# Optimization experiments

Hardware: AMD Instinct MI355X
Metric: run time of the kernel (lower is better)

## Reference

```python
import jax, jax.numpy as jnp
import numpy as np

TLEN, BSZ, HID = 64, 32, 1024
SLEN = 200
V_TGT = 32000
V_EXT = 2000
UNK = 0  # ext_dict UNK index, ignored in the onehot scatter


def setup_inputs() -> dict:
    key = jax.random.key(0)
    ks = jax.random.split(key, 6)
    hidden = jax.random.normal(ks[0], (TLEN, BSZ, HID), dtype=jnp.float32)
    attn = jax.random.uniform(ks[1], (TLEN, BSZ, SLEN), dtype=jnp.float32)
    attn = attn / jnp.sum(attn, axis=-1, keepdims=True)  # attention-like distribution
    copy_to_ext = jax.random.randint(ks[2], (SLEN, BSZ), 0, V_EXT)
    W_out = jax.random.normal(ks[3], (V_TGT, HID), dtype=jnp.float32) * 0.02
    b_out = jnp.zeros((V_TGT,), dtype=jnp.float32)
    w_copy = jax.random.normal(ks[4], (1, HID), dtype=jnp.float32) * 0.02
    b_copy = jnp.zeros((1,), dtype=jnp.float32)
    return {"hidden": hidden, "attn": attn, "copy_to_ext": copy_to_ext,
            "W_out": W_out, "b_out": b_out, "w_copy": w_copy, "b_copy": b_copy}


def _safe_log(v):
    return jnp.log(jnp.clip(v, 0.001, 1.0 - 0.001))


def reference(hidden, attn, copy_to_ext, W_out, b_out, w_copy, b_copy):
    tlen, bsz, hid = hidden.shape
    slen = attn.shape[-1]
    h = hidden.reshape(tlen * bsz, hid)
    a = attn.reshape(tlen * bsz, slen)

    # p(copy) gate
    copy = jax.nn.sigmoid(h @ w_copy.T + b_copy)            # [N, 1]
    # generator log-probs over tgt vocab
    logits = h @ W_out.T + b_out                            # [N, V_TGT]
    prob_log = jax.nn.log_softmax(logits, axis=-1)
    out_prob_log = prob_log + _safe_log(copy)

    # attention mass scaled by (1 - p(copy)) -- NOTE: matches source exactly
    mul_attn = a * (1.0 - copy)                             # [N, SLEN]
    mul_attn_b = mul_attn.reshape(tlen, bsz, slen).transpose(1, 0, 2)  # [B, T, S]
    idx = copy_to_ext.T                                     # [B, S]

    def per_batch(m, i):
        # m: [T, S], i: [S]; scatter-add attn mass into ext vocab, ignoring UNK
        valid = (i != UNK).astype(m.dtype)                  # onehot ignore_index
        return jax.ops.segment_sum((m * valid).T, i, num_segments=V_EXT).T  # [T, E]

    ext_copy_prob = jax.vmap(per_batch)(mul_attn_b, idx)    # [B, T, E]
    ext_copy_prob = ext_copy_prob.transpose(1, 0, 2).reshape(tlen * bsz, V_EXT)
    ext_copy_prob_log = _safe_log(ext_copy_prob)

    out = jnp.concatenate([out_prob_log, ext_copy_prob_log], axis=1)
    return out.reshape(tlen, bsz, V_TGT + V_EXT)
```

## Files before the change

kernel.cpp:

```cpp
#include <hip/hip_runtime.h>
#include <cstdint>
#include <cstddef>

#define TLEN 64
#define BSZ  32
#define NROW 2048
#define HID  1024
#define SLEN 200
#define VT   32000
#define VE   2000
#define OUTW 34000

typedef float  f32x4  __attribute__((ext_vector_type(4)));
typedef __bf16 bf16x4 __attribute__((ext_vector_type(4)));
typedef __bf16 bf16x8 __attribute__((ext_vector_type(8)));
typedef float  floatx4 __attribute__((ext_vector_type(4)));

__global__ void cvt_kernel(const float* __restrict__ src, __bf16* __restrict__ dst, int n4) {
  int i = blockIdx.x * blockDim.x + threadIdx.x;
  int stride = gridDim.x * blockDim.x;
  for (; i < n4; i += stride) {
    f32x4 v = ((const f32x4*)src)[i];
    bf16x4 o;
    o.x = (__bf16)v.x; o.y = (__bf16)v.y; o.z = (__bf16)v.z; o.w = (__bf16)v.w;
    ((bf16x4*)dst)[i] = o;
  }
}

__global__ __launch_bounds__(256) void gate_kernel(
    const float* __restrict__ h, const float* __restrict__ wc,
    const float* __restrict__ bc,
    float* __restrict__ logcopy, float* __restrict__ oneminus) {
  int row = blockIdx.x;
  int tid = threadIdx.x;
  const float* hr = h + (size_t)row * HID;
  float s = 0.f;
  for (int k = tid; k < HID; k += 256) s += hr[k] * wc[k];
  #pragma unroll
  for (int off = 32; off; off >>= 1) s += __shfl_down(s, off, 64);
  __shared__ float wsum[4];
  int lane = tid & 63, w = tid >> 6;
  if (lane == 0) wsum[w] = s;
  __syncthreads();
  if (tid == 0) {
    float x = wsum[0] + wsum[1] + wsum[2] + wsum[3] + bc[0];
    float pc = 1.f / (1.f + __expf(-x));
    float pcc = fminf(fmaxf(pc, 0.001f), 0.999f);
    logcopy[row]  = logf(pcc);
    oneminus[row] = 1.f - pc;
  }
}

#define BM 128
#define BN 128
#define BK 32

__device__ __forceinline__ void load_lds16(const __bf16* g, __bf16* s) {
  __builtin_amdgcn_global_load_lds(
      (const __attribute__((address_space(1))) void*)g,
      (__attribute__((address_space(3))) void*)s, 16, 0, 0);
}

__global__ __launch_bounds__(256) void gemm_kernel(
    const __bf16* __restrict__ A, const __bf16* __restrict__ B,
    const float* __restrict__ bias, float* __restrict__ out) {
  __shared__ __attribute__((aligned(16))) __bf16 As[BM * BK];
  __shared__ __attribute__((aligned(16))) __bf16 Bs[BN * BK];

  const int tid = threadIdx.x;
  const int bn = blockIdx.x;
  const int bm = blockIdx.y;
  const int K = HID;

  const __bf16* aptr0 = A + (size_t)(bm * BM + (tid >> 2)) * K + (tid & 3) * 8;
  const __bf16* aptr1 = aptr0 + (size_t)64 * K;
  const __bf16* bptr0 = B + (size_t)(bn * BN + (tid >> 2)) * K + (tid & 3) * 8;
  const __bf16* bptr1 = bptr0 + (size_t)64 * K;
  __bf16* alds0 = &As[tid * 8];
  __bf16* alds1 = &As[2048 + tid * 8];
  __bf16* blds0 = &Bs[tid * 8];
  __bf16* blds1 = &Bs[2048 + tid * 8];

  const int l  = tid & 63;
  const int w  = tid >> 6;
  const int wm = w & 1;
  const int wn = w >> 1;
  const int lr = l & 15;
  const int q  = l >> 4;

  const bf16x8* Asv = (const bf16x8*)As;
  const bf16x8* Bsv = (const bf16x8*)Bs;

  int aidx[4], bidx[4];
  #pragma unroll
  for (int i = 0; i < 4; i++) aidx[i] = (wm * 64 + i * 16 + lr) * 4 + q;
  #pragma unroll
  for (int j = 0; j < 4; j++) bidx[j] = (wn * 64 + j * 16 + lr) * 4 + q;

  floatx4 acc[4][4] = {};

  for (int kt = 0; kt < K; kt += BK) {
    load_lds16(aptr0 + kt, alds0);
    load_lds16(aptr1 + kt, alds1);
    load_lds16(bptr0 + kt, blds0);
    load_lds16(bptr1 + kt, blds1);
    __syncthreads();

    bf16x8 af[4], bfr[4];
    #pragma unroll
    for (int i = 0; i < 4; i++) af[i] = Asv[aidx[i]];
    #pragma unroll
    for (int j = 0; j < 4; j++) bfr[j] = Bsv[bidx[j]];

    #pragma unroll
    for (int i = 0; i < 4; i++)
      #pragma unroll
      for (int j = 0; j < 4; j++)
        acc[i][j] = __builtin_amdgcn_mfma_f32_16x16x32_bf16(af[i], bfr[j], acc[i][j], 0, 0, 0);

    __syncthreads();
  }

  const int col0 = bn * BN + wn * 64 + lr;
  const int row0 = bm * BM + wm * 64 + q * 4;
  float bv[4];
  #pragma unroll
  for (int j = 0; j < 4; j++) bv[j] = bias[col0 + j * 16];
  #pragma unroll
  for (int i = 0; i < 4; i++) {
    #pragma unroll
    for (int r = 0; r < 4; r++) {
      int m = row0 + i * 16 + r;
      float* po = out + (size_t)m * OUTW + col0;
      #pragma unroll
      for (int j = 0; j < 4; j++)
        po[j * 16] = acc[i][j][r] + bv[j];
    }
  }
}

__global__ __launch_bounds__(256) void lse_kernel(
    const float* __restrict__ out, const float* __restrict__ logcopy,
    float* __restrict__ sub) {
  int row = blockIdx.x;
  int tid = threadIdx.x;
  const float* p = out + (size_t)row * OUTW;

  float mx = -3.0e38f, sm = 0.f;
  for (int k2 = 0; k2 < 31; k2++) {
    f32x4 v = *(const f32x4*)(p + 4 * (tid + k2 * 256));
    #pragma unroll
    for (int e = 0; e < 4; e++) {
      float x = v[e];
      float nm = fmaxf(mx, x);
      sm = sm * __expf(mx - nm) + __expf(x - nm);
      mx = nm;
    }
  }
  {
    float x = p[31744 + tid];
    float nm = fmaxf(mx, x);
    sm = sm * __expf(mx - nm) + __expf(x - nm);
    mx = nm;
  }
  #pragma unroll
  for (int off = 32; off; off >>= 1) {
    float om = __shfl_down(mx, off, 64);
    float os = __shfl_down(sm, off, 64);
    float nm = fmaxf(mx, om);
    sm = sm * __expf(mx - nm) + os * __expf(om - nm);
    mx = nm;
  }
  __shared__ float sx_[4], sm_[4];
  int lane = tid & 63, w = tid >> 6;
  if (lane == 0) { sx_[w] = mx; sm_[w] = sm; }
  __syncthreads();
  if (tid == 0) {
    float M = sx_[0], S = sm_[0];
    #pragma unroll
    for (int i = 1; i < 4; i++) {
      float nm = fmaxf(M, sx_[i]);
      S = S * __expf(M - nm) + sm_[i] * __expf(sx_[i] - nm);
      M = nm;
    }
    sub[row] = M + logf(S) - logcopy[row];
  }
}

__global__ __launch_bounds__(256) void fix_kernel(float* __restrict__ out,
                                                 const float* __restrict__ sub) {
  int row = blockIdx.y;
  int i = blockIdx.x * 256 + threadIdx.x;
  if (i < VT / 4) {
    float sv = sub[row];
    f32x4* p = (f32x4*)(out + (size_t)row * OUTW) + i;
    f32x4 v = *p;
    v = v - sv;
    *p = v;
  }
}

__global__ __launch_bounds__(256) void ext_kernel(
    const float* __restrict__ attn, const int* __restrict__ c2e,
    const float* __restrict__ oneminus, float* __restrict__ out) {
  __shared__ float ext[VE];
  int row = blockIdx.x;
  int b = row & (BSZ - 1);
  int tid = threadIdx.x;
  for (int e = tid; e < VE; e += 256) ext[e] = 0.f;
  __syncthreads();
  float om = oneminus[row];
  if (tid < SLEN) {
    int idx = c2e[tid * BSZ + b];
    if (idx != 0)
      atomicAdd(&ext[idx], attn[(size_t)row * SLEN + tid] * om);
  }
  __syncthreads();
  float* op = out + (size_t)row * OUTW + VT;
  for (int e = tid; e < VE; e += 256)
    op[e] = logf(fminf(fmaxf(ext[e], 0.001f), 0.999f));
}

extern "C" void kernel_launch(void* const* d_in, const int* in_sizes, int n_in,
                              void* d_out, int out_size, void* d_ws, size_t ws_size,
                              hipStream_t stream) {
  const float* hidden = (const float*)d_in[0];
  const float* attn   = (const float*)d_in[1];
  const int*   c2e    = (const int*)d_in[2];
  const float* W      = (const float*)d_in[3];
  const float* bout   = (const float*)d_in[4];
  const float* wc     = (const float*)d_in[5];
  const float* bc     = (const float*)d_in[6];
  float* out = (float*)d_out;

  char* ws = (char*)d_ws;
  __bf16* Hbf = (__bf16*)ws;
  __bf16* Wbf = (__bf16*)(ws + 4194304);
  float* logcopy  = (float*)(ws + 4194304 + 65536000);
  float* oneminus = logcopy + NROW;
  float* sub      = oneminus + NROW;

  cvt_kernel<<<1024, 256, 0, stream>>>(hidden, Hbf, (NROW * HID) / 4);
  cvt_kernel<<<4096, 256, 0, stream>>>(W, Wbf, (VT * HID) / 4);
  gate_kernel<<<NROW, 256, 0, stream>>>(hidden, wc, bc, logcopy, oneminus);
  gemm_kernel<<<dim3(VT / BN, NROW / BM), 256, 0, stream>>>(Hbf, Wbf, bout, out);
  lse_kernel<<<NROW, 256, 0, stream>>>(out, logcopy, sub);
  fix_kernel<<<dim3(32, NROW), 256, 0, stream>>>(out, sub);
  ext_kernel<<<NROW, 256, 0, stream>>>(attn, c2e, oneminus, out);
}
```

Before: 698.7 us.

## Fuse softmax partial reduction into GEMM epilogue and merge finishing passes

The GEMM epilogue now computes a per-tile row max and sum-of-exponents. It stores these partials as float2 pairs in the not-yet-written ext-vocab region of each output row. A single finish kernel combines the partials into the log-sum-exp, subtracts it from the logits in place, and does the copy scatter and log for the ext vocab. This replaces the separate lse, fix and ext kernels. The hidden-state bf16 conversion is folded into the gate kernel. Together these remove one full read pass over the large logits matrix and two kernel launches, at the cost of extra shuffles and exps in the GEMM epilogue.

Result: no change. 696.9 us (-0.3%).

```diff
diff --git a/kernel.cpp b/kernel.cpp
--- a/kernel.cpp
+++ b/kernel.cpp
@@ -10,6 +10,7 @@
 #define VT   32000
 #define VE   2000
 #define OUTW 34000
+#define NBN  250
 
 typedef float  f32x4  __attribute__((ext_vector_type(4)));
 typedef __bf16 bf16x4 __attribute__((ext_vector_type(4)));
@@ -29,13 +30,16 @@
 
 __global__ __launch_bounds__(256) void gate_kernel(
     const float* __restrict__ h, const float* __restrict__ wc,
-    const float* __restrict__ bc,
+    const float* __restrict__ bc, __bf16* __restrict__ Hbf,
     float* __restrict__ logcopy, float* __restrict__ oneminus) {
   int row = blockIdx.x;
   int tid = threadIdx.x;
-  const float* hr = h + (size_t)row * HID;
-  float s = 0.f;
-  for (int k = tid; k < HID; k += 256) s += hr[k] * wc[k];
+  f32x4 v  = ((const f32x4*)(h + (size_t)row * HID))[tid];
+  f32x4 wv = ((const f32x4*)wc)[tid];
+  bf16x4 o;
+  o.x = (__bf16)v.x; o.y = (__bf16)v.y; o.z = (__bf16)v.z; o.w = (__bf16)v.w;
+  ((bf16x4*)(Hbf + (size_t)row * HID))[tid] = o;
+  float s = v.x * wv.x + v.y * wv.y + v.z * wv.z + v.w * wv.w;
   #pragma unroll
   for (int off = 32; off; off >>= 1) s += __shfl_down(s, off, 64);
   __shared__ float wsum[4];
@@ -66,6 +70,7 @@
     const float* __restrict__ bias, float* __restrict__ out) {
   __shared__ __attribute__((aligned(16))) __bf16 As[BM * BK];
   __shared__ __attribute__((aligned(16))) __bf16 Bs[BN * BK];
+  __shared__ float lM0[128], lS0[128], lM1[128], lS1[128];
 
   const int tid = threadIdx.x;
   const int bn = blockIdx.x;
@@ -126,99 +131,102 @@
   float bv[4];
   #pragma unroll
   for (int j = 0; j < 4; j++) bv[j] = bias[col0 + j * 16];
+
   #pragma unroll
   for (int i = 0; i < 4; i++) {
     #pragma unroll
     for (int r = 0; r < 4; r++) {
       int m = row0 + i * 16 + r;
       float* po = out + (size_t)m * OUTW + col0;
-      #pragma unroll
-      for (int j = 0; j < 4; j++)
-        po[j * 16] = acc[i][j][r] + bv[j];
+      float vj[4];
+      #pragma unroll
+      for (int j = 0; j < 4; j++) vj[j] = acc[i][j][r] + bv[j];
+      #pragma unroll
+      for (int j = 0; j < 4; j++) po[j * 16] = vj[j];
+      float m4 = fmaxf(fmaxf(vj[0], vj[1]), fmaxf(vj[2], vj[3]));
+      #pragma unroll
+      for (int off = 1; off < 16; off <<= 1) m4 = fmaxf(m4, __shfl_xor(m4, off, 64));
+      float s4 = __expf(vj[0] - m4) + __expf(vj[1] - m4) +
+                 __expf(vj[2] - m4) + __expf(vj[3] - m4);
+      #pragma unroll
+      for (int off = 1; off < 16; off <<= 1) s4 += __shfl_xor(s4, off, 64);
+      if (lr == 0) {
+        int rl = wm * 64 + i * 16 + q * 4 + r;
+        if (wn == 0) { lM0[rl] = m4; lS0[rl] = s4; }
+        else         { lM1[rl] = m4; lS1[rl] = s4; }
+      }
     }
   }
-}
-
-__global__ __launch_bounds__(256) void lse_kernel(
-    const float* __restrict__ out, const float* __restrict__ logcopy,
-    float* __restrict__ sub) {
+  __syncthreads();
+  if (w == 0) {
+    for (int e = l; e < 128; e += 64) {
+      float Ma = lM0[e], Sa = lS0[e], Mb = lM1[e], Sb = lS1[e];
+      float nm = fmaxf(Ma, Mb);
+      float Sc = Sa * __expf(Ma - nm) + Sb * __expf(Mb - nm);
+      int m = bm * BM + e;
+      float2* pp = (float2*)(out + (size_t)m * OUTW + VT);
+      pp[bn] = make_float2(nm, Sc);
+    }
+  }
+}
+
+__global__ __launch_bounds__(256) void finish_kernel(
+    const float* __restrict__ attn, const int* __restrict__ c2e,
+    const float* __restrict__ logcopy, const float* __restrict__ oneminus,
+    float* __restrict__ out) {
+  __shared__ float ext[VE];
+  __shared__ float rM[4], rS[4];
   int row = blockIdx.x;
   int tid = threadIdx.x;
-  const float* p = out + (size_t)row * OUTW;
-
-  float mx = -3.0e38f, sm = 0.f;
-  for (int k2 = 0; k2 < 31; k2++) {
-    f32x4 v = *(const f32x4*)(p + 4 * (tid + k2 * 256));
-    #pragma unroll
-    for (int e = 0; e < 4; e++) {
-      float x = v[e];
-      float nm = fmaxf(mx, x);
-      sm = sm * __expf(mx - nm) + __expf(x - nm);
-      mx = nm;
-    }
-  }
-  {
-    float x = p[31744 + tid];
-    float nm = fmaxf(mx, x);
-    sm = sm * __expf(mx - nm) + __expf(x - nm);
-    mx = nm;
+  int b = row & (BSZ - 1);
+  float* orow = out + (size_t)row * OUTW;
+
+  for (int e = tid; e < VE; e += 256) ext[e] = 0.f;
+
+  float M = -3.0e38f, S = 0.f;
+  if (tid < NBN) {
+    float2 p = ((const float2*)(orow + VT))[tid];
+    M = p.x; S = p.y;
   }
   #pragma unroll
   for (int off = 32; off; off >>= 1) {
-    float om = __shfl_down(mx, off, 64);
-    float os = __shfl_down(sm, off, 64);
-    float nm = fmaxf(mx, om);
-    sm = sm * __expf(mx - nm) + os * __expf(om - nm);
-    mx = nm;
-  }
-  __shared__ float sx_[4], sm_[4];
+    float om = __shfl_down(M, off, 64);
+    float os = __shfl_down(S, off, 64);
+    float nm = fmaxf(M, om);
+    S = S * __expf(M - nm) + os * __expf(om - nm);
+    M = nm;
+  }
   int lane = tid & 63, w = tid >> 6;
-  if (lane == 0) { sx_[w] = mx; sm_[w] = sm; }
-  __syncthreads();
-  if (tid == 0) {
-    float M = sx_[0], S = sm_[0];
-    #pragma unroll
-    for (int i = 1; i < 4; i++) {
-      float nm = fmaxf(M, sx_[i]);
-      S = S * __expf(M - nm) + sm_[i] * __expf(sx_[i] - nm);
-      M = nm;
-    }
-    sub[row] = M + logf(S) - logcopy[row];
-  }
-}
-
-__global__ __launch_bounds__(256) void fix_kernel(float* __restrict__ out,
-                                                 const float* __restrict__ sub) {
-  int row = blockIdx.y;
-  int i = blockIdx.x * 256 + threadIdx.x;
-  if (i < VT / 4) {
-    float sv = sub[row];
-    f32x4* p = (f32x4*)(out + (size_t)row * OUTW) + i;
-    f32x4 v = *p;
-    v = v - sv;
-    *p = v;
-  }
-}
-
-__global__ __launch_bounds__(256) void ext_kernel(
-    const float* __restrict__ attn, const int* __restrict__ c2e,
-    const float* __restrict__ oneminus, float* __restrict__ out) {
-  __shared__ float ext[VE];
-  int row = blockIdx.x;
-  int b = row & (BSZ - 1);
-  int tid = threadIdx.x;
-  for (int e = tid; e < VE; e += 256) ext[e] = 0.f;
-  __syncthreads();
-  float om = oneminus[row];
+  if (lane == 0) { rM[w] = M; rS[w] = S; }
+  __syncthreads();
+  float Mf = rM[0], Sf = rS[0];
+  #pragma unroll
+  for (int i = 1; i < 4; i++) {
+    float nm = fmaxf(Mf, rM[i]);
+    Sf = Sf * __expf(Mf - nm) + rS[i] * __expf(rM[i] - nm);
+    Mf = nm;
+  }
+  float sub = Mf + logf(Sf) - logcopy[row];
+
+  float om1 = oneminus[row];
   if (tid < SLEN) {
     int idx = c2e[tid * BSZ + b];
     if (idx != 0)
-      atomicAdd(&ext[idx], attn[(size_t)row * SLEN + tid] * om);
-  }
-  __syncthreads();
-  float* op = out + (size_t)row * OUTW + VT;
+      atomicAdd(&ext[idx], attn[(size_t)row * SLEN + tid] * om1);
+  }
+
+  #pragma unroll 4
+  for (int k2 = 0; k2 < 31; k2++) {
+    f32x4* p = (f32x4*)orow + (tid + k2 * 256);
+    f32x4 v = *p;
+    v = v - sub;
+    *p = v;
+  }
+  orow[31744 + tid] -= sub;
+
+  __syncthreads();
   for (int e = tid; e < VE; e += 256)
-    op[e] = logf(fminf(fmaxf(ext[e], 0.001f), 0.999f));
+    orow[VT + e] = logf(fminf(fmaxf(ext[e], 0.001f), 0.999f));
 }
 
 extern "C" void kernel_launch(void* const* d_in, const int* in_sizes, int n_in,
@@ -238,13 +246,9 @@
   __bf16* Wbf = (__bf16*)(ws + 4194304);
   float* logcopy  = (float*)(ws + 4194304 + 65536000);
   float* oneminus = logcopy + NROW;
-  float* sub      = oneminus + NROW;
-
-  cvt_kernel<<<1024, 256, 0, stream>>>(hidden, Hbf, (NROW * HID) / 4);
+
   cvt_kernel<<<4096, 256, 0, stream>>>(W, Wbf, (VT * HID) / 4);
-  gate_kernel<<<NROW, 256, 0, stream>>>(hidden, wc, bc, logcopy, oneminus);
+  gate_kernel<<<NROW, 256, 0, stream>>>(hidden, wc, bc, Hbf, logcopy, oneminus);
   gemm_kernel<<<dim3(VT / BN, NROW / BM), 256, 0, stream>>>(Hbf, Wbf, bout, out);
-  lse_kernel<<<NROW, 256, 0, stream>>>(out, logcopy, sub);
-  fix_kernel<<<dim3(32, NROW), 256, 0, stream>>>(out, sub);
-  ext_kernel<<<NROW, 256, 0, stream>>>(attn, c2e, oneminus, out);
-}
+  finish_kernel<<<NROW, 256, 0, stream>>>(attn, c2e, logcopy, oneminus, out);
+}
```
